# Kernel tuning notes

Measured on AMD Instinct MI355X. Metric: run time of the kernel, lower is better.

Reference implementation:

```python
import jax, jax.numpy as jnp
import numpy as np

BOUND = 1.0
MIN_NEAR = 0.5
NUM_STEPS = 64
UPSAMPLE_STEPS = 64
HIDDEN = 64


def near_far_cube(rays_o, rays_d):
    # AABB [-BOUND, BOUND]^3 slab intersection, faithful to near_far_from_bound(type='cube')
    tmin = (-BOUND - rays_o) / (rays_d + 1e-15)
    tmax = (BOUND - rays_o) / (rays_d + 1e-15)
    near = jnp.minimum(tmin, tmax).max(axis=-1, keepdims=True)
    far = jnp.maximum(tmin, tmax).min(axis=-1, keepdims=True)
    miss = far < near
    near = jnp.where(miss, 1e9, near)
    far = jnp.where(miss, 1e9, far)
    near = jnp.maximum(near, MIN_NEAR)
    return near, far


def sample_pdf(bins, weights, n_samples):
    # bins: [B,Q,N,T], weights: [B,Q,N,T-1]; deterministic (det=True, eval mode)
    B, Q, N, T = bins.shape
    M = B * Q * N
    bins = bins.reshape(M, T)
    w = weights.reshape(M, -1) + 1e-5
    pdf = w / jnp.sum(w, axis=-1, keepdims=True)
    cdf = jnp.cumsum(pdf, axis=-1)
    cdf = jnp.concatenate([jnp.zeros_like(cdf[..., :1]), cdf], axis=-1)  # [M, T]
    u = jnp.linspace(0.5 / n_samples, 1.0 - 0.5 / n_samples, n_samples, dtype=bins.dtype)
    u = jnp.broadcast_to(u, (M, n_samples))
    inds = jax.vmap(lambda c, uu: jnp.searchsorted(c, uu, side='right'))(cdf, u)
    Tc = cdf.shape[-1]
    below = jnp.maximum(inds - 1, 0)
    above = jnp.minimum(inds, Tc - 1)
    cdf0 = jnp.take_along_axis(cdf, below, axis=-1)
    cdf1 = jnp.take_along_axis(cdf, above, axis=-1)
    bins0 = jnp.take_along_axis(bins, below, axis=-1)
    bins1 = jnp.take_along_axis(bins, above, axis=-1)
    denom = cdf1 - cdf0
    denom = jnp.where(denom < 1e-5, jnp.ones_like(denom), denom)
    t = (u - cdf0) / denom
    samples = bins0 + t * (bins1 - bins0)
    return samples.reshape(B, Q, N, n_samples)


def density_fn(x, W1, b1, w_sigma, b_sigma):
    h = jax.nn.relu(x @ W1 + b1)
    return jax.nn.softplus(h @ w_sigma + b_sigma)  # [..., 1]


def color_fn(x, d, Wc1, bc1, Wc2, bc2):
    h = jax.nn.relu(jnp.concatenate([x, d], axis=-1) @ Wc1 + bc1)
    return jax.nn.sigmoid(h @ Wc2 + bc2)  # [..., 3]


def composite_weights(z_vals, sigma, sample_dist):
    deltas = z_vals[..., 1:] - z_vals[..., :-1]
    deltas = jnp.concatenate([deltas, sample_dist * jnp.ones_like(deltas[..., :1])], axis=-1)
    alphas = 1.0 - jnp.exp(-deltas * sigma[..., 0])
    shifted = jnp.concatenate([jnp.ones_like(alphas[..., :1]), 1.0 - alphas + 1e-15], axis=-1)
    weights = alphas * jnp.cumprod(shifted, axis=-1)[..., :-1]
    return weights, deltas


def reference(rays_o, rays_d, W1, b1, w_sigma, b_sigma, Wc1, bc1, Wc2, bc2):
    nears, fars = near_far_cube(rays_o, rays_d)            # [B,Q,N,1]
    z = jnp.linspace(0.0, 1.0, NUM_STEPS, dtype=rays_o.dtype)
    z_vals = nears + (fars - nears) * z                    # [B,Q,N,S]
    sample_dist = (fars - nears) / NUM_STEPS               # [B,Q,N,1]
    xyzs = rays_o[..., None, :] + rays_d[..., None, :] * z_vals[..., None]
    sigma = density_fn(xyzs, W1, b1, w_sigma, b_sigma)     # [B,Q,N,S,1]

    # hierarchical importance sampling (no_grad in original)
    w_coarse, deltas_c = composite_weights(z_vals, sigma, sample_dist)
    z_mid = z_vals[..., :-1] + 0.5 * deltas_c[..., :-1]
    new_z = jax.lax.stop_gradient(sample_pdf(z_mid, w_coarse[..., 1:-1], UPSAMPLE_STEPS))
    new_xyzs = rays_o[..., None, :] + rays_d[..., None, :] * new_z[..., None]
    new_sigma = density_fn(new_xyzs, W1, b1, w_sigma, b_sigma)

    # merge and resort samples along ray
    z_all = jnp.concatenate([z_vals, new_z], axis=-1)
    z_index = jnp.argsort(z_all, axis=-1)
    z_all = jnp.take_along_axis(z_all, z_index, axis=-1)
    xyz_all = jnp.concatenate([xyzs, new_xyzs], axis=-2)
    xyz_all = jnp.take_along_axis(xyz_all, jnp.broadcast_to(z_index[..., None], xyz_all.shape), axis=-2)
    sig_all = jnp.concatenate([sigma, new_sigma], axis=-2)
    sig_all = jnp.take_along_axis(sig_all, jnp.broadcast_to(z_index[..., None], sig_all.shape), axis=-2)

    weights, _ = composite_weights(z_all, sig_all, sample_dist)   # [B,Q,N,2S]
    dirs = jnp.broadcast_to(rays_d[..., None, :], xyz_all.shape)
    rgbs = color_fn(xyz_all, dirs, Wc1, bc1, Wc2, bc2)            # [B,Q,N,2S,3]

    weights_sum = weights.sum(axis=-1)
    image = jnp.sum(weights[..., None] * rgbs, axis=-2)
    image = image + (1.0 - weights_sum)[..., None] * 1.0          # bg_radius==0 -> bg_color=1
    return image                                                  # [B,Q,N,3]


def setup_inputs() -> dict:
    key = jax.random.key(0)
    ks = jax.random.split(key, 12)
    B, Q, N = 1, 4, 4096
    o = jax.random.normal(ks[0], (B, Q, N, 3), dtype=jnp.float32)
    rays_o = 2.5 * o / (jnp.linalg.norm(o, axis=-1, keepdims=True) + 1e-8)
    d = -rays_o + 0.1 * jax.random.normal(ks[1], (B, Q, N, 3), dtype=jnp.float32)
    rays_d = d / (jnp.linalg.norm(d, axis=-1, keepdims=True) + 1e-8)
    return {
        'rays_o': rays_o,
        'rays_d': rays_d,
        'W1': jax.random.normal(ks[2], (3, HIDDEN), dtype=jnp.float32) * 0.5,
        'b1': jax.random.normal(ks[3], (HIDDEN,), dtype=jnp.float32) * 0.1,
        'w_sigma': jax.random.normal(ks[4], (HIDDEN, 1), dtype=jnp.float32) * 0.3,
        'b_sigma': jax.random.normal(ks[5], (1,), dtype=jnp.float32) * 0.1,
        'Wc1': jax.random.normal(ks[6], (6, HIDDEN), dtype=jnp.float32) * 0.5,
        'bc1': jax.random.normal(ks[7], (HIDDEN,), dtype=jnp.float32) * 0.1,
        'Wc2': jax.random.normal(ks[8], (HIDDEN, 3), dtype=jnp.float32) * 0.3,
        'bc2': jax.random.normal(ks[9], (3,), dtype=jnp.float32) * 0.1,
    }
```

## Files before the change

kernel.cpp:

```cpp
#include <hip/hip_runtime.h>
#include <math.h>


#define EXP2F(x) __builtin_amdgcn_exp2f(x)
#define LOG2F(x) __builtin_amdgcn_logf(x)
#define RCPF(x)  __builtin_amdgcn_rcpf(x)
#define WSYNC()  __builtin_amdgcn_wave_barrier()

typedef float f32x2 __attribute__((ext_vector_type(2)));

__device__ __forceinline__ f32x2 pk_fma(f32x2 a, f32x2 b, f32x2 c) {
    return __builtin_elementwise_fma(a, b, c);
}
__device__ __forceinline__ f32x2 pk_relu(f32x2 a) {
    const f32x2 z2 = {0.0f, 0.0f};
    return __builtin_elementwise_max(a, z2);
}

union F4 { float4 v; f32x2 h[2]; };

__device__ __forceinline__ float fast_exp(float x)   { return EXP2F(x * 1.44269504088896340736f); }
__device__ __forceinline__ float fast_sigmoid(float x) { return RCPF(1.0f + EXP2F(-x * 1.44269504088896340736f)); }
__device__ __forceinline__ float fast_softplus(float x) {
    float y = EXP2F(-fabsf(x) * 1.44269504088896340736f);
    return fmaxf(x, 0.0f) + 0.6931471805599453f * LOG2F(1.0f + y);
}

struct __align__(16) RayLds {
    float dA[64];
    float dB[64];
    float dw[64];
    float cA[64];
    float cB[64];
    float cwr[64];
    float cwg[64];
    float cwb[64];
    float z[64];
    float nz[64];
    float cdf[64];
    float bins[64];
    float zall[128];
    float sall[128];
};

__device__ __forceinline__ int count_lt(const float* __restrict__ arr, float key) {
    int c = 0;
    #pragma unroll
    for (int s = 32; s >= 1; s >>= 1)
        c += (arr[c + s - 1] < key) ? s : 0;
    c += (arr[c] < key) ? 1 : 0;
    return c;
}
__device__ __forceinline__ int count_le(const float* __restrict__ arr, float key) {
    int c = 0;
    #pragma unroll
    for (int s = 32; s >= 1; s >>= 1)
        c += (arr[c + s - 1] <= key) ? s : 0;
    c += (arr[c] <= key) ? 1 : 0;
    return c;
}

__device__ __forceinline__ float density_eval(float zv, const RayLds& R, float bsig) {
    const float4* A4 = (const float4*)R.dA;
    const float4* B4 = (const float4*)R.dB;
    const float4* W4 = (const float4*)R.dw;
    const f32x2 z2 = {zv, zv};
    const f32x2 zero2 = {0.0f, 0.0f};
    f32x2 acc0 = zero2, acc1 = zero2, acc2 = zero2, acc3 = zero2;
    #pragma unroll
    for (int g = 0; g < 16; g += 2) {
        F4 a0, b0, w0, a1, b1, w1;
        a0.v = A4[g];     b0.v = B4[g];     w0.v = W4[g];
        a1.v = A4[g + 1]; b1.v = B4[g + 1]; w1.v = W4[g + 1];
        acc0 = pk_fma(pk_relu(pk_fma(z2, b0.h[0], a0.h[0])), w0.h[0], acc0);
        acc1 = pk_fma(pk_relu(pk_fma(z2, b0.h[1], a0.h[1])), w0.h[1], acc1);
        acc2 = pk_fma(pk_relu(pk_fma(z2, b1.h[0], a1.h[0])), w1.h[0], acc2);
        acc3 = pk_fma(pk_relu(pk_fma(z2, b1.h[1], a1.h[1])), w1.h[1], acc3);
    }
    float s = ((acc0.x + acc0.y) + (acc1.x + acc1.y))
            + ((acc2.x + acc2.y) + (acc3.x + acc3.y));
    return fast_softplus(s + bsig);
}

__global__ __launch_bounds__(256) void nerf_render_kernel(
    const float* __restrict__ rays_o, const float* __restrict__ rays_d,
    const float* __restrict__ W1, const float* __restrict__ b1,
    const float* __restrict__ w_sigma, const float* __restrict__ b_sigma,
    const float* __restrict__ Wc1, const float* __restrict__ bc1,
    const float* __restrict__ Wc2, const float* __restrict__ bc2,
    float* __restrict__ out, int nrays)
{
    __shared__ RayLds L[4];
    const int wave = threadIdx.x >> 6;
    const int lane = threadIdx.x & 63;
    int ray = blockIdx.x * 4 + wave;
    const bool valid = ray < nrays;
    if (!valid) ray = 0;
    RayLds& R = L[wave];

    const float ox = rays_o[ray * 3 + 0], oy = rays_o[ray * 3 + 1], oz = rays_o[ray * 3 + 2];
    const float dx = rays_d[ray * 3 + 0], dy = rays_d[ray * 3 + 1], dz = rays_d[ray * 3 + 2];
    const float bsig = b_sigma[0];
    const float bc2r = bc2[0], bc2g = bc2[1], bc2b = bc2[2];

    {
        const int j = lane;
        float w0 = W1[j], w1 = W1[64 + j], w2 = W1[128 + j];
        R.dA[j] = fmaf(ox, w0, fmaf(oy, w1, fmaf(oz, w2, b1[j])));
        R.dB[j] = fmaf(dx, w0, fmaf(dy, w1, dz * w2));
        R.dw[j] = w_sigma[j];

        float c0 = Wc1[j], c1 = Wc1[64 + j], c2 = Wc1[128 + j];
        float c3 = Wc1[192 + j], c4 = Wc1[256 + j], c5 = Wc1[320 + j];
        R.cA[j] = fmaf(ox, c0, fmaf(oy, c1, fmaf(oz, c2,
                  fmaf(dx, c3, fmaf(dy, c4, fmaf(dz, c5, bc1[j]))))));
        R.cB[j] = fmaf(dx, c0, fmaf(dy, c1, dz * c2));
        R.cwr[j] = Wc2[3 * j + 0];
        R.cwg[j] = Wc2[3 * j + 1];
        R.cwb[j] = Wc2[3 * j + 2];
    }

    float ivx = RCPF(dx + 1e-15f), ivy = RCPF(dy + 1e-15f), ivz = RCPF(dz + 1e-15f);
    float tax = (-1.0f - ox) * ivx, tbx = (1.0f - ox) * ivx;
    float tay = (-1.0f - oy) * ivy, tby = (1.0f - oy) * ivy;
    float taz = (-1.0f - oz) * ivz, tbz = (1.0f - oz) * ivz;
    float nearv = fmaxf(fmaxf(fminf(tax, tbx), fminf(tay, tby)), fminf(taz, tbz));
    float farv  = fminf(fminf(fmaxf(tax, tbx), fmaxf(tay, tby)), fmaxf(taz, tbz));
    if (farv < nearv) { nearv = 1e9f; farv = 1e9f; }
    nearv = fmaxf(nearv, 0.5f);
    const float sample_dist = (farv - nearv) * (1.0f / 64.0f);
    const float step = (farv - nearv) * (1.0f / 63.0f);

    WSYNC();

    const float z = fmaf((float)lane, step, nearv);
    const float sig = density_eval(z, R, bsig);
    R.z[lane] = z;

    float delta = (lane < 63) ? step : sample_dist;
    float e = fast_exp(-delta * sig);
    float alpha = 1.0f - e;
    float T = e + 1e-15f;

    float pincl = T;
    #pragma unroll
    for (int off = 1; off < 64; off <<= 1) {
        float v = __shfl_up(pincl, off);
        if (lane >= off) pincl *= v;
    }
    float pexcl = __shfl_up(pincl, 1);
    if (lane == 0) pexcl = 1.0f;
    const float wgt = alpha * pexcl;

    float val = (lane >= 1 && lane <= 62) ? (wgt + 1e-5f) : 0.0f;
    float sincl = val;
    #pragma unroll
    for (int off = 1; off < 64; off <<= 1) {
        float v = __shfl_up(sincl, off);
        if (lane >= off) sincl += v;
    }
    const float rws = RCPF(__shfl(sincl, 63));
    R.cdf[lane]  = sincl * rws;
    R.bins[lane] = fmaf(0.5f, step, z);
    WSYNC();

    const float u = ((float)lane + 0.5f) * (1.0f / 64.0f);
    int ind = count_le(R.cdf, u);
    int below = max(ind - 1, 0);
    int above = min(ind, 62);
    float cdf0 = R.cdf[below], cdf1 = R.cdf[above];
    float bin0 = R.bins[below], bin1 = R.bins[above];
    float denom = cdf1 - cdf0;
    if (denom < 1e-5f) denom = 1.0f;
    float t = (u - cdf0) * RCPF(denom);
    const float nz = fmaf(t, bin1 - bin0, bin0);

    const float nsig = density_eval(nz, R, bsig);
    R.nz[lane] = nz;
    WSYNC();

    int posO = lane + count_lt(R.nz, z);
    int posN = lane + count_le(R.z, nz);
    R.zall[posO] = z;   R.sall[posO] = sig;
    R.zall[posN] = nz;  R.sall[posN] = nsig;
    WSYNC();

    float2 zz = ((const float2*)R.zall)[lane];
    float2 ss = ((const float2*)R.sall)[lane];
    float za = zz.x, zb = zz.y;
    float zc = __shfl_down(za, 1);
    float d0 = zb - za;
    float d1 = (lane < 63) ? (zc - zb) : sample_dist;
    float ea = fast_exp(-d0 * ss.x), eb = fast_exp(-d1 * ss.y);
    float a0 = 1.0f - ea, a1 = 1.0f - eb;
    float T0 = ea + 1e-15f, T1 = eb + 1e-15f;

    float ppin = T0 * T1;
    #pragma unroll
    for (int off = 1; off < 64; off <<= 1) {
        float v = __shfl_up(ppin, off);
        if (lane >= off) ppin *= v;
    }
    const float prodAll = __shfl(ppin, 63);
    float pex = __shfl_up(ppin, 1);
    if (lane == 0) pex = 1.0f;
    float w0 = a0 * pex;
    float w1 = a1 * pex * T0;

    const float4* CA4 = (const float4*)R.cA;
    const float4* CB4 = (const float4*)R.cB;
    const float4* WR4 = (const float4*)R.cwr;
    const float4* WG4 = (const float4*)R.cwg;
    const float4* WB4 = (const float4*)R.cwb;
    const f32x2 zero2 = {0.0f, 0.0f};
    const f32x2 za2 = {za, za}, zb2 = {zb, zb};
    f32x2 ar0 = zero2, ag0 = zero2, ab0 = zero2;
    f32x2 ar1 = zero2, ag1 = zero2, ab1 = zero2;
    #pragma unroll
    for (int g = 0; g < 16; ++g) {
        F4 a, b, wr, wg, wb;
        a.v = CA4[g]; b.v = CB4[g];
        wr.v = WR4[g]; wg.v = WG4[g]; wb.v = WB4[g];
        f32x2 h0l = pk_relu(pk_fma(za2, b.h[0], a.h[0]));
        f32x2 h0h = pk_relu(pk_fma(za2, b.h[1], a.h[1]));
        f32x2 h1l = pk_relu(pk_fma(zb2, b.h[0], a.h[0]));
        f32x2 h1h = pk_relu(pk_fma(zb2, b.h[1], a.h[1]));
        ar0 = pk_fma(h0l, wr.h[0], ar0); ar0 = pk_fma(h0h, wr.h[1], ar0);
        ag0 = pk_fma(h0l, wg.h[0], ag0); ag0 = pk_fma(h0h, wg.h[1], ag0);
        ab0 = pk_fma(h0l, wb.h[0], ab0); ab0 = pk_fma(h0h, wb.h[1], ab0);
        ar1 = pk_fma(h1l, wr.h[0], ar1); ar1 = pk_fma(h1h, wr.h[1], ar1);
        ag1 = pk_fma(h1l, wg.h[0], ag1); ag1 = pk_fma(h1h, wg.h[1], ag1);
        ab1 = pk_fma(h1l, wb.h[0], ab1); ab1 = pk_fma(h1h, wb.h[1], ab1);
    }
    float r0 = fast_sigmoid(ar0.x + ar0.y + bc2r);
    float g0 = fast_sigmoid(ag0.x + ag0.y + bc2g);
    float c0 = fast_sigmoid(ab0.x + ab0.y + bc2b);
    float r1 = fast_sigmoid(ar1.x + ar1.y + bc2r);
    float g1 = fast_sigmoid(ag1.x + ag1.y + bc2g);
    float c1 = fast_sigmoid(ab1.x + ab1.y + bc2b);

    float accR = w0 * r0 + w1 * r1;
    float accG = w0 * g0 + w1 * g1;
    float accB = w0 * c0 + w1 * c1;
    #pragma unroll
    for (int off = 32; off > 0; off >>= 1) {
        accR += __shfl_xor(accR, off);
        accG += __shfl_xor(accG, off);
        accB += __shfl_xor(accB, off);
    }
    if (lane == 0 && valid) {
        out[ray * 3 + 0] = accR + prodAll;
        out[ray * 3 + 1] = accG + prodAll;
        out[ray * 3 + 2] = accB + prodAll;
    }
}

extern "C" void kernel_launch(void* const* d_in, const int* in_sizes, int n_in,
                              void* d_out, int out_size, void* d_ws, size_t ws_size,
                              hipStream_t stream) {
    const float* rays_o  = (const float*)d_in[0];
    const float* rays_d  = (const float*)d_in[1];
    const float* W1      = (const float*)d_in[2];
    const float* b1      = (const float*)d_in[3];
    const float* w_sigma = (const float*)d_in[4];
    const float* b_sigma = (const float*)d_in[5];
    const float* Wc1     = (const float*)d_in[6];
    const float* bc1     = (const float*)d_in[7];
    const float* Wc2     = (const float*)d_in[8];
    const float* bc2     = (const float*)d_in[9];
    float* out = (float*)d_out;

    int nrays = in_sizes[0] / 3;
    int blocks = (nrays + 3) / 4;
    nerf_render_kernel<<<blocks, 256, 0, stream>>>(
        rays_o, rays_d, W1, b1, w_sigma, b_sigma, Wc1, bc1, Wc2, bc2, out, nrays);
}
```

Measured before the change: 103.5 us.

## Use DPP wavefront scans and move shared weights from LDS to uniform global

Replaces the shuffle-based prefix product/sum scans and the final xor reductions with DPP row-shift/broadcast scans plus readlane. The exclusive product is recovered by dividing by the lane's own value. A small setup kernel transposes the ray-independent weights (Wc2, w_sigma) into workspace, so they are read straight from global memory instead of being copied into LDS for each ray. This cuts LDS traffic and shuffle latency. The cost is an extra kernel launch, and the divide-based exclusive scan could lose accuracy when transmittance values underflow.

```diff
diff --git a/kernel.cpp b/kernel.cpp
--- a/kernel.cpp
+++ b/kernel.cpp
@@ -18,6 +18,32 @@
 }
 
 union F4 { float4 v; f32x2 h[2]; };
+
+#define DPPF(x, ctrl, old, rmask) \
+    __int_as_float(__builtin_amdgcn_update_dpp( \
+        __float_as_int(old), __float_as_int(x), (ctrl), (rmask), 0xf, false))
+
+__device__ __forceinline__ float scan_mul(float x) {
+    x *= DPPF(x, 0x111, 1.0f, 0xf);
+    x *= DPPF(x, 0x112, 1.0f, 0xf);
+    x *= DPPF(x, 0x114, 1.0f, 0xf);
+    x *= DPPF(x, 0x118, 1.0f, 0xf);
+    x *= DPPF(x, 0x142, 1.0f, 0xa);
+    x *= DPPF(x, 0x143, 1.0f, 0xc);
+    return x;
+}
+__device__ __forceinline__ float scan_add(float x) {
+    x += DPPF(x, 0x111, 0.0f, 0xf);
+    x += DPPF(x, 0x112, 0.0f, 0xf);
+    x += DPPF(x, 0x114, 0.0f, 0xf);
+    x += DPPF(x, 0x118, 0.0f, 0xf);
+    x += DPPF(x, 0x142, 0.0f, 0xa);
+    x += DPPF(x, 0x143, 0.0f, 0xc);
+    return x;
+}
+__device__ __forceinline__ float lane63(float x) {
+    return __int_as_float(__builtin_amdgcn_readlane(__float_as_int(x), 63));
+}
 
 __device__ __forceinline__ float fast_exp(float x)   { return EXP2F(x * 1.44269504088896340736f); }
 __device__ __forceinline__ float fast_sigmoid(float x) { return RCPF(1.0f + EXP2F(-x * 1.44269504088896340736f)); }
@@ -29,12 +55,8 @@
 struct __align__(16) RayLds {
     float dA[64];
     float dB[64];
-    float dw[64];
     float cA[64];
     float cB[64];
-    float cwr[64];
-    float cwg[64];
-    float cwb[64];
     float z[64];
     float nz[64];
     float cdf[64];
@@ -60,10 +82,11 @@
     return c;
 }
 
-__device__ __forceinline__ float density_eval(float zv, const RayLds& R, float bsig) {
+__device__ __forceinline__ float density_eval(float zv, const RayLds& R,
+                                              const float* __restrict__ wT, float bsig) {
     const float4* A4 = (const float4*)R.dA;
     const float4* B4 = (const float4*)R.dB;
-    const float4* W4 = (const float4*)R.dw;
+    const float4* W4 = (const float4*)(wT + 192);
     const f32x2 z2 = {zv, zv};
     const f32x2 zero2 = {0.0f, 0.0f};
     f32x2 acc0 = zero2, acc1 = zero2, acc2 = zero2, acc3 = zero2;
@@ -82,12 +105,23 @@
     return fast_softplus(s + bsig);
 }
 
+__global__ void setup_weights(const float* __restrict__ w_sigma,
+                              const float* __restrict__ Wc2,
+                              float* __restrict__ wT) {
+    const int j = threadIdx.x;
+    wT[j]       = Wc2[3 * j + 0];
+    wT[64 + j]  = Wc2[3 * j + 1];
+    wT[128 + j] = Wc2[3 * j + 2];
+    wT[192 + j] = w_sigma[j];
+}
+
 __global__ __launch_bounds__(256) void nerf_render_kernel(
     const float* __restrict__ rays_o, const float* __restrict__ rays_d,
     const float* __restrict__ W1, const float* __restrict__ b1,
-    const float* __restrict__ w_sigma, const float* __restrict__ b_sigma,
+    const float* __restrict__ b_sigma,
     const float* __restrict__ Wc1, const float* __restrict__ bc1,
-    const float* __restrict__ Wc2, const float* __restrict__ bc2,
+    const float* __restrict__ bc2,
+    const float* __restrict__ wT,
     float* __restrict__ out, int nrays)
 {
     __shared__ RayLds L[4];
@@ -108,16 +142,12 @@
         float w0 = W1[j], w1 = W1[64 + j], w2 = W1[128 + j];
         R.dA[j] = fmaf(ox, w0, fmaf(oy, w1, fmaf(oz, w2, b1[j])));
         R.dB[j] = fmaf(dx, w0, fmaf(dy, w1, dz * w2));
-        R.dw[j] = w_sigma[j];
 
         float c0 = Wc1[j], c1 = Wc1[64 + j], c2 = Wc1[128 + j];
         float c3 = Wc1[192 + j], c4 = Wc1[256 + j], c5 = Wc1[320 + j];
         R.cA[j] = fmaf(ox, c0, fmaf(oy, c1, fmaf(oz, c2,
                   fmaf(dx, c3, fmaf(dy, c4, fmaf(dz, c5, bc1[j]))))));
         R.cB[j] = fmaf(dx, c0, fmaf(dy, c1, dz * c2));
-        R.cwr[j] = Wc2[3 * j + 0];
-        R.cwg[j] = Wc2[3 * j + 1];
-        R.cwb[j] = Wc2[3 * j + 2];
     }
 
     float ivx = RCPF(dx + 1e-15f), ivy = RCPF(dy + 1e-15f), ivz = RCPF(dz + 1e-15f);
@@ -134,7 +164,7 @@
     WSYNC();
 
     const float z = fmaf((float)lane, step, nearv);
-    const float sig = density_eval(z, R, bsig);
+    const float sig = density_eval(z, R, wT, bsig);
     R.z[lane] = z;
 
     float delta = (lane < 63) ? step : sample_dist;
@@ -142,24 +172,13 @@
     float alpha = 1.0f - e;
     float T = e + 1e-15f;
 
-    float pincl = T;
-    #pragma unroll
-    for (int off = 1; off < 64; off <<= 1) {
-        float v = __shfl_up(pincl, off);
-        if (lane >= off) pincl *= v;
-    }
-    float pexcl = __shfl_up(pincl, 1);
-    if (lane == 0) pexcl = 1.0f;
+    float pincl = scan_mul(T);
+    float pexcl = pincl * RCPF(T);
     const float wgt = alpha * pexcl;
 
     float val = (lane >= 1 && lane <= 62) ? (wgt + 1e-5f) : 0.0f;
-    float sincl = val;
-    #pragma unroll
-    for (int off = 1; off < 64; off <<= 1) {
-        float v = __shfl_up(sincl, off);
-        if (lane >= off) sincl += v;
-    }
-    const float rws = RCPF(__shfl(sincl, 63));
+    float sincl = scan_add(val);
+    const float rws = RCPF(lane63(sincl));
     R.cdf[lane]  = sincl * rws;
     R.bins[lane] = fmaf(0.5f, step, z);
     WSYNC();
@@ -175,7 +194,7 @@
     float t = (u - cdf0) * RCPF(denom);
     const float nz = fmaf(t, bin1 - bin0, bin0);
 
-    const float nsig = density_eval(nz, R, bsig);
+    const float nsig = density_eval(nz, R, wT, bsig);
     R.nz[lane] = nz;
     WSYNC();
 
@@ -195,23 +214,18 @@
     float a0 = 1.0f - ea, a1 = 1.0f - eb;
     float T0 = ea + 1e-15f, T1 = eb + 1e-15f;
 
-    float ppin = T0 * T1;
-    #pragma unroll
-    for (int off = 1; off < 64; off <<= 1) {
-        float v = __shfl_up(ppin, off);
-        if (lane >= off) ppin *= v;
-    }
-    const float prodAll = __shfl(ppin, 63);
-    float pex = __shfl_up(ppin, 1);
-    if (lane == 0) pex = 1.0f;
+    float P = T0 * T1;
+    float ppin = scan_mul(P);
+    const float prodAll = lane63(ppin);
+    float pex = ppin * RCPF(P);
     float w0 = a0 * pex;
     float w1 = a1 * pex * T0;
 
     const float4* CA4 = (const float4*)R.cA;
     const float4* CB4 = (const float4*)R.cB;
-    const float4* WR4 = (const float4*)R.cwr;
-    const float4* WG4 = (const float4*)R.cwg;
-    const float4* WB4 = (const float4*)R.cwb;
+    const float4* WR4 = (const float4*)(wT);
+    const float4* WG4 = (const float4*)(wT + 64);
+    const float4* WB4 = (const float4*)(wT + 128);
     const f32x2 zero2 = {0.0f, 0.0f};
     const f32x2 za2 = {za, za}, zb2 = {zb, zb};
     f32x2 ar0 = zero2, ag0 = zero2, ab0 = zero2;
@@ -239,19 +253,14 @@
     float g1 = fast_sigmoid(ag1.x + ag1.y + bc2g);
     float c1 = fast_sigmoid(ab1.x + ab1.y + bc2b);
 
-    float accR = w0 * r0 + w1 * r1;
-    float accG = w0 * g0 + w1 * g1;
-    float accB = w0 * c0 + w1 * c1;
-    #pragma unroll
-    for (int off = 32; off > 0; off >>= 1) {
-        accR += __shfl_xor(accR, off);
-        accG += __shfl_xor(accG, off);
-        accB += __shfl_xor(accB, off);
-    }
+    float totR = lane63(scan_add(w0 * r0 + w1 * r1));
+    float totG = lane63(scan_add(w0 * g0 + w1 * g1));
+    float totB = lane63(scan_add(w0 * c0 + w1 * c1));
+
     if (lane == 0 && valid) {
-        out[ray * 3 + 0] = accR + prodAll;
-        out[ray * 3 + 1] = accG + prodAll;
-        out[ray * 3 + 2] = accB + prodAll;
+        out[ray * 3 + 0] = totR + prodAll;
+        out[ray * 3 + 1] = totG + prodAll;
+        out[ray * 3 + 2] = totB + prodAll;
     }
 }
 
@@ -269,9 +278,12 @@
     const float* Wc2     = (const float*)d_in[8];
     const float* bc2     = (const float*)d_in[9];
     float* out = (float*)d_out;
+    float* wT  = (float*)d_ws;
+
+    setup_weights<<<1, 64, 0, stream>>>(w_sigma, Wc2, wT);
 
     int nrays = in_sizes[0] / 3;
     int blocks = (nrays + 3) / 4;
     nerf_render_kernel<<<blocks, 256, 0, stream>>>(
-        rays_o, rays_d, W1, b1, w_sigma, b_sigma, Wc1, bc1, Wc2, bc2, out, nrays);
-}
+        rays_o, rays_d, W1, b1, b_sigma, Wc1, bc1, bc2, wT, out, nrays);
+}
```

Measured after the change: 101.7 us. No clear change (-1.7%).
